# Kernel optimization log

Hardware: AMD Instinct MI355X
Metric: run time of the kernel (lower is better)

## Reference

```python
import jax, jax.numpy as jnp
import numpy as np

N_NODES = 50000
N_GRAPHS = 128
HEADS = 10
F_XD = 78


def _linear(x, W, b):
    return x @ W + b


def _conv1d(x, w, b):
    # x: [B, Cin, L], w: [Cout, Cin, K]
    y = jax.lax.conv_general_dilated(x, w, (1,), 'VALID',
                                     dimension_numbers=('NCH', 'OIH', 'NCH'))
    return y + b[None, :, None]


def _add_self_loops(src, dst, n):
    loop = jnp.arange(n, dtype=src.dtype)
    return jnp.concatenate([src, loop]), jnp.concatenate([dst, loop])


def _gat_conv(x, src, dst, W, att_src, att_dst, b, n):
    # PyG GATConv, concat heads, self-loops, negative_slope=0.2
    h = (x @ W).reshape(n, HEADS, F_XD)               # [N,H,F]
    a_s = jnp.sum(h * att_src[None], axis=-1)          # [N,H]
    a_d = jnp.sum(h * att_dst[None], axis=-1)          # [N,H]
    e = jax.nn.leaky_relu(a_s[src] + a_d[dst], 0.2)    # [E,H]
    m = jax.ops.segment_max(e, dst, num_segments=n)    # [N,H]
    m = jnp.where(jnp.isfinite(m), m, 0.0)
    ex = jnp.exp(e - m[dst])
    s = jax.ops.segment_sum(ex, dst, num_segments=n)
    alpha = ex / (s[dst] + 1e-16)                      # [E,H]
    out = jax.ops.segment_sum(h[src] * alpha[:, :, None], dst, num_segments=n)
    return out.reshape(n, HEADS * F_XD) + b


def _gcn_conv(x, src, dst, W, b, n):
    # PyG GCNConv: self-loops + symmetric normalization
    h = x @ W                                          # [N,C]
    ones = jnp.ones(src.shape[0], dtype=h.dtype)
    deg = jax.ops.segment_sum(ones, dst, num_segments=n)
    dinv = jnp.where(deg > 0, jax.lax.rsqrt(deg), 0.0)
    norm = dinv[src] * dinv[dst]                       # [E]
    out = jax.ops.segment_sum(h[src] * norm[:, None], dst, num_segments=n)
    return out + b


def _forward(x, edge_index, batch, target1, target2, params):
    p = params
    n = x.shape[0]
    src0, dst0 = edge_index[0], edge_index[1]
    src, dst = _add_self_loops(src0, dst0, n)

    h = jax.nn.relu(_gat_conv(x, src, dst, p['W_gat'], p['att_src'], p['att_dst'], p['b_gat'], n))
    h = jax.nn.relu(_gcn_conv(h, src, dst, p['W_gcn'], p['b_gcn'], n))

    # global max + mean pool per graph
    cnt = jax.ops.segment_sum(jnp.ones(n, dtype=h.dtype), batch, num_segments=N_GRAPHS)
    gmx = jax.ops.segment_max(h, batch, num_segments=N_GRAPHS)
    gmx = jnp.where(cnt[:, None] > 0, gmx, 0.0)
    gav = jax.ops.segment_sum(h, batch, num_segments=N_GRAPHS) / jnp.maximum(cnt, 1.0)[:, None]
    g = jnp.concatenate([gmx, gav], axis=1)            # [B,1560]

    g = jax.nn.relu(_linear(g, p['W_fcg1'], p['b_fcg1']))  # dropout = identity (eval)
    g = _linear(g, p['W_fcg2'], p['b_fcg2'])               # [B,128]

    # protein branch 2: embedding + conv1d over embed dim
    emb = p['emb'][target2]                            # [B,1000,128]
    xt2 = _conv1d(emb, p['Wc2'], p['bc2'])             # [B,32,121]
    xt2 = _linear(xt2.reshape(xt2.shape[0], 32 * 121), p['W_fc2xt'], p['b_fc2xt'])

    # protein branch 1: conv1d on raw float features
    xt1 = _conv1d(target1, p['Wc1'], p['bc1'])         # [B,32,17]
    xt1 = _linear(xt1.reshape(xt1.shape[0], 544), p['W_fc1xt'], p['b_fc1xt'])

    xc = jnp.concatenate([g, xt1, xt2], axis=1)        # [B,384]
    xc = jax.nn.relu(_linear(xc, p['W_fc1'], p['b_fc1']))
    xc = jax.nn.relu(_linear(xc, p['W_fc2'], p['b_fc2']))
    return _linear(xc, p['W_out'], p['b_out'])         # [B,1]


def setup_inputs() -> dict:
    key = jax.random.key(0)
    ks = jax.random.split(key, 32)

    def w(k, shape, fan_in):
        return jax.random.normal(k, shape, dtype=jnp.float32) * (1.0 / np.sqrt(fan_in))

    inp = {}
    inp['x'] = jax.random.normal(ks[0], (N_NODES, F_XD), dtype=jnp.float32)
    inp['edge_index'] = jax.random.randint(ks[1], (2, 150000), 0, N_NODES, dtype=jnp.int64) if jax.config.jax_enable_x64 else jax.random.randint(ks[1], (2, 150000), 0, N_NODES).astype(jnp.int32)
    inp['batch'] = jnp.sort(jax.random.randint(ks[2], (N_NODES,), 0, N_GRAPHS)).astype(jnp.int32)
    inp['target1'] = jax.random.normal(ks[3], (N_GRAPHS, 20, 24), dtype=jnp.float32)
    inp['target2'] = jax.random.randint(ks[4], (N_GRAPHS, 1000), 0, 26).astype(jnp.int32)

    inp['W_gat'] = w(ks[5], (F_XD, HEADS * F_XD), F_XD)
    inp['att_src'] = w(ks[6], (HEADS, F_XD), F_XD)
    inp['att_dst'] = w(ks[7], (HEADS, F_XD), F_XD)
    inp['b_gat'] = jnp.zeros((HEADS * F_XD,), jnp.float32)
    inp['W_gcn'] = w(ks[8], (780, 780), 780)
    inp['b_gcn'] = jnp.zeros((780,), jnp.float32)
    inp['W_fcg1'] = w(ks[9], (1560, 1500), 1560)
    inp['b_fcg1'] = jnp.zeros((1500,), jnp.float32)
    inp['W_fcg2'] = w(ks[10], (1500, 128), 1500)
    inp['b_fcg2'] = jnp.zeros((128,), jnp.float32)
    inp['emb'] = jax.random.normal(ks[11], (26, 128), dtype=jnp.float32)
    inp['Wc2'] = w(ks[12], (32, 1000, 8), 1000 * 8)
    inp['bc2'] = jnp.zeros((32,), jnp.float32)
    inp['W_fc2xt'] = w(ks[13], (32 * 121, 128), 32 * 121)
    inp['b_fc2xt'] = jnp.zeros((128,), jnp.float32)
    inp['Wc1'] = w(ks[14], (32, 20, 8), 20 * 8)
    inp['bc1'] = jnp.zeros((32,), jnp.float32)
    inp['W_fc1xt'] = w(ks[15], (544, 128), 544)
    inp['b_fc1xt'] = jnp.zeros((128,), jnp.float32)
    inp['W_fc1'] = w(ks[16], (384, 1024), 384)
    inp['b_fc1'] = jnp.zeros((1024,), jnp.float32)
    inp['W_fc2'] = w(ks[17], (1024, 512), 1024)
    inp['b_fc2'] = jnp.zeros((512,), jnp.float32)
    inp['W_out'] = w(ks[18], (512, 1), 512)
    inp['b_out'] = jnp.zeros((1,), jnp.float32)
    return inp


def reference(x, edge_index, batch, target1, target2,
              W_gat, att_src, att_dst, b_gat, W_gcn, b_gcn,
              W_fcg1, b_fcg1, W_fcg2, b_fcg2, emb, Wc2, bc2,
              W_fc2xt, b_fc2xt, Wc1, bc1, W_fc1xt, b_fc1xt,
              W_fc1, b_fc1, W_fc2, b_fc2, W_out, b_out):
    params = dict(W_gat=W_gat, att_src=att_src, att_dst=att_dst, b_gat=b_gat,
                  W_gcn=W_gcn, b_gcn=b_gcn, W_fcg1=W_fcg1, b_fcg1=b_fcg1,
                  W_fcg2=W_fcg2, b_fcg2=b_fcg2, emb=emb, Wc2=Wc2, bc2=bc2,
                  W_fc2xt=W_fc2xt, b_fc2xt=b_fc2xt, Wc1=Wc1, bc1=bc1,
                  W_fc1xt=W_fc1xt, b_fc1xt=b_fc1xt, W_fc1=W_fc1, b_fc1=b_fc1,
                  W_fc2=W_fc2, b_fc2=b_fc2, W_out=W_out, b_out=b_out)
    return _forward(x, edge_index, batch, target1, target2, params)
```

## Files before the change

### kernel.cpp

```cpp
#include <hip/hip_runtime.h>
#include <cstdio>
#include <cstdint>

#define CDIV(a,b) (((a)+(b)-1)/(b))

static const int N   = 50000;
static const int NE0 = 150000;
static const int NE  = 200000;
static const int H   = 10;
static const int F   = 78;
static const int C   = 780;
static const int G   = 128;
static const int KP_GAT = 96;
static const int XAGG_LD = 960;
static const int CP1 = 800;
static const int CP1A = 832;
static const int CP2 = 784;
static const int POOL_SPLIT = 8;
static const int BM_SPLIT = 4;

typedef __attribute__((ext_vector_type(8))) short bf16x8;
typedef __attribute__((ext_vector_type(4))) float f32x4;
typedef __attribute__((ext_vector_type(8))) unsigned short us8;

__device__ __forceinline__ float bf2f(unsigned short u) {
    return __uint_as_float(((unsigned int)u) << 16);
}
__device__ __forceinline__ unsigned short f2bf(float f) {
    unsigned int u = __float_as_uint(f);
    u = (u + 0x7fff + ((u >> 16) & 1)) >> 16;
    return (unsigned short)u;
}

__device__ __forceinline__ void async16(const unsigned short* g, unsigned short* l) {
    __builtin_amdgcn_global_load_lds(
        (const __attribute__((address_space(1))) unsigned int*)g,
        (__attribute__((address_space(3))) unsigned int*)l, 16, 0, 0);
}

__global__ __launch_bounds__(256)
void gemm_mfma64(const unsigned short* __restrict__ A,
                 const unsigned short* __restrict__ Bt,
                 unsigned short* __restrict__ Cb,
                 const float* __restrict__ bias, int relu,
                 int M, int Nn, int kSteps, int lda, int ldb, int ldc, int nct)
{
    __shared__ unsigned short As[128][64];
    __shared__ unsigned short Bs[128][64];
    const int tid  = threadIdx.x;
    const int lane = tid & 63;
    const int wave = tid >> 6;
    const int wm = (wave >> 1) * 64, wn = (wave & 1) * 64;

    const int nwg = gridDim.x;
    const int q8 = nwg >> 3, r8 = nwg & 7;
    const int xcd = blockIdx.x & 7, sub = blockIdx.x >> 3;
    const int wg = (xcd < r8) ? xcd * (q8 + 1) + sub
                              : r8 * (q8 + 1) + (xcd - r8) * q8 + sub;
    const int bm = (wg / nct) * 128, bn = (wg % nct) * 128;

    f32x4 acc[4][4] = {};

    const int mrow = lane & 15, quad = lane >> 4;
    const int srow = wave * 8 + (lane >> 3);
    const int segoff = ((lane & 7) ^ (lane >> 3)) * 8;

    const unsigned short* gA[4];
    const unsigned short* gB[4];
    unsigned short* lA[4];
    unsigned short* lB[4];
#pragma unroll
    for (int c = 0; c < 4; c++) {
        int r = c * 32 + srow;
        gA[c] = A  + (size_t)min(bm + r, M - 1)  * lda + segoff;
        gB[c] = Bt + (size_t)min(bn + r, Nn - 1) * ldb + segoff;
        lA[c] = &As[c * 32 + wave * 8][0];
        lB[c] = &Bs[c * 32 + wave * 8][0];
    }

    for (int ks = 0; ks < kSteps; ks++) {
        const int k0 = ks * 64;
#pragma unroll
        for (int c = 0; c < 4; c++) async16(gA[c] + k0, lA[c]);
#pragma unroll
        for (int c = 0; c < 4; c++) async16(gB[c] + k0, lB[c]);
        __syncthreads();
#pragma unroll
        for (int kk = 0; kk < 2; kk++) {
            bf16x8 af[4], bfr[4];
#pragma unroll
            for (int i = 0; i < 4; i++) {
                int ra = wm + i * 16 + mrow;
                af[i]  = *(const bf16x8*)&As[ra][(((kk * 4 + quad) ^ (ra & 7))) * 8];
                int rb = wn + i * 16 + mrow;
                bfr[i] = *(const bf16x8*)&Bs[rb][(((kk * 4 + quad) ^ (rb & 7))) * 8];
            }
#pragma unroll
            for (int i = 0; i < 4; i++)
#pragma unroll
                for (int j = 0; j < 4; j++)
                    acc[i][j] = __builtin_amdgcn_mfma_f32_16x16x32_bf16(af[i], bfr[j], acc[i][j], 0, 0, 0);
        }
        __syncthreads();
    }

#pragma unroll
    for (int i = 0; i < 4; i++) {
#pragma unroll
        for (int j = 0; j < 4; j++) {
            int col = bn + wn + j * 16 + mrow;
            if (col >= Nn) continue;
            float bv = bias ? bias[col] : 0.f;
#pragma unroll
            for (int r = 0; r < 4; r++) {
                int row = bm + wm + i * 16 + quad * 4 + r;
                if (row >= M) continue;
                float v = acc[i][j][r] + bv;
                if (relu) v = fmaxf(v, 0.f);
                Cb[(size_t)row * ldc + col] = f2bf(v);
            }
        }
    }
}

__global__ __launch_bounds__(256)
void gemm_gat(const unsigned short* __restrict__ A,
              const unsigned short* __restrict__ Bt,
              const float* __restrict__ bias,
              unsigned short* __restrict__ Cb)
{
    __shared__ unsigned short As[128][32];
    __shared__ unsigned short Bs[128][32];
    const int tid  = threadIdx.x;
    const int lane = tid & 63;
    const int wave = tid >> 6;
    const int wm = (wave >> 1) * 64, wn = (wave & 1) * 64;
    const int h = blockIdx.y;

    const int nwg = gridDim.x;
    const int q8 = nwg >> 3, r8 = nwg & 7;
    const int xcd = blockIdx.x & 7, sub = blockIdx.x >> 3;
    const int wg = (xcd < r8) ? xcd * (q8 + 1) + sub
                              : r8 * (q8 + 1) + (xcd - r8) * q8 + sub;
    const int bm = wg * 128;

    f32x4 acc[4][4] = {};

    const int mrow = lane & 15, quad = lane >> 4;
    const int subr = lane >> 2;
    const int segp = ((lane & 3) ^ ((lane >> 3) & 3)) * 8;
    const int segr = (quad ^ ((mrow >> 1) & 3)) * 8;

    const unsigned short* gA0 = A + (size_t)min(bm + wave * 16 + subr,      N - 1) * XAGG_LD + h * KP_GAT + segp;
    const unsigned short* gA1 = A + (size_t)min(bm + 64 + wave * 16 + subr, N - 1) * XAGG_LD + h * KP_GAT + segp;
    const unsigned short* gB0 = Bt + (size_t)(h * 80 + min(wave * 16 + subr,      79)) * KP_GAT + segp;
    const unsigned short* gB1 = Bt + (size_t)(h * 80 + min(64 + wave * 16 + subr, 79)) * KP_GAT + segp;
    unsigned short* lA0 = &As[wave * 16][0];
    unsigned short* lA1 = &As[64 + wave * 16][0];
    unsigned short* lB0 = &Bs[wave * 16][0];
    unsigned short* lB1 = &Bs[64 + wave * 16][0];

#pragma unroll
    for (int ks = 0; ks < 3; ks++) {
        const int k0 = ks * 32;
        async16(gA0 + k0, lA0);
        async16(gA1 + k0, lA1);
        async16(gB0 + k0, lB0);
        async16(gB1 + k0, lB1);
        __syncthreads();
        bf16x8 af[4], bfr[4];
#pragma unroll
        for (int i = 0; i < 4; i++) {
            af[i]  = *(const bf16x8*)&As[wm + i * 16 + mrow][segr];
            bfr[i] = *(const bf16x8*)&Bs[wn + i * 16 + mrow][segr];
        }
#pragma unroll
        for (int i = 0; i < 4; i++)
#pragma unroll
            for (int j = 0; j < 4; j++)
                acc[i][j] = __builtin_amdgcn_mfma_f32_16x16x32_bf16(af[i], bfr[j], acc[i][j], 0, 0, 0);
        __syncthreads();
    }

#pragma unroll
    for (int i = 0; i < 4; i++) {
#pragma unroll
        for (int j = 0; j < 4; j++) {
            int cl = wn + j * 16 + mrow;
            if (cl >= 80) continue;
            float bv = bias[h * 80 + cl];
#pragma unroll
            for (int r = 0; r < 4; r++) {
                int row = bm + wm + i * 16 + quad * 4 + r;
                if (row >= N) continue;
                float v = fmaxf(acc[i][j][r] + bv, 0.f);
                Cb[(size_t)row * CP1A + h * 80 + cl] = f2bf(v);
            }
        }
    }
}

__global__ __launch_bounds__(256)
void gemm_mfma_sk(const unsigned short* __restrict__ A,
                  const unsigned short* __restrict__ Bt,
                  float* __restrict__ Cp,
                  int M, int Nn, int kSteps, int lda, int ldb, int nct)
{
    __shared__ unsigned short As[128][32];
    __shared__ unsigned short Bs[128][32];
    const int tid  = threadIdx.x;
    const int lane = tid & 63;
    const int wave = tid >> 6;
    const int wm = (wave >> 1) * 64, wn = (wave & 1) * 64;
    const int bm = (blockIdx.x / nct) * 128, bn = (blockIdx.x % nct) * 128;

    const int split = blockIdx.y, KS = gridDim.y;
    const int per = CDIV(kSteps, KS);
    const int kb = split * per;
    const int ke = min(kb + per, kSteps);

    f32x4 acc[4][4] = {};

    const int mrow = lane & 15, quad = lane >> 4;
    const int subr = lane >> 2;
    const int segp = ((lane & 3) ^ ((lane >> 3) & 3)) * 8;
    const int segr = (quad ^ ((mrow >> 1) & 3)) * 8;

    const unsigned short* gA0 = A  + (size_t)min(bm + wave * 16 + subr,      M - 1)  * lda + segp;
    const unsigned short* gA1 = A  + (size_t)min(bm + 64 + wave * 16 + subr, M - 1)  * lda + segp;
    const unsigned short* gB0 = Bt + (size_t)min(bn + wave * 16 + subr,      Nn - 1) * ldb + segp;
    const unsigned short* gB1 = Bt + (size_t)min(bn + 64 + wave * 16 + subr, Nn - 1) * ldb + segp;
    unsigned short* lA0 = &As[wave * 16][0];
    unsigned short* lA1 = &As[64 + wave * 16][0];
    unsigned short* lB0 = &Bs[wave * 16][0];
    unsigned short* lB1 = &Bs[64 + wave * 16][0];

    for (int ks = kb; ks < ke; ks++) {
        const int k0 = ks * 32;
        async16(gA0 + k0, lA0);
        async16(gA1 + k0, lA1);
        async16(gB0 + k0, lB0);
        async16(gB1 + k0, lB1);
        __syncthreads();
        bf16x8 af[4], bfr[4];
#pragma unroll
        for (int i = 0; i < 4; i++) {
            af[i]  = *(const bf16x8*)&As[wm + i * 16 + mrow][segr];
            bfr[i] = *(const bf16x8*)&Bs[wn + i * 16 + mrow][segr];
        }
#pragma unroll
        for (int i = 0; i < 4; i++)
#pragma unroll
            for (int j = 0; j < 4; j++)
                acc[i][j] = __builtin_amdgcn_mfma_f32_16x16x32_bf16(af[i], bfr[j], acc[i][j], 0, 0, 0);
        __syncthreads();
    }

    float* Cs = Cp + (size_t)split * M * Nn;
#pragma unroll
    for (int i = 0; i < 4; i++) {
#pragma unroll
        for (int j = 0; j < 4; j++) {
            int col = bn + wn + j * 16 + mrow;
            if (col >= Nn) continue;
#pragma unroll
            for (int r = 0; r < 4; r++) {
                int row = bm + wm + i * 16 + quad * 4 + r;
                if (row >= M) continue;
                Cs[(size_t)row * Nn + col] = acc[i][j][r];
            }
        }
    }
}

__global__ void k_sk_reduce(const float* __restrict__ Cp, int KS, int M, int Nn,
                            const float* __restrict__ bias, int relu,
                            unsigned short* __restrict__ Cb, int ldc)
{
    int idx = blockIdx.x * blockDim.x + threadIdx.x;
    if (idx >= M * Nn) return;
    int row = idx / Nn, col = idx % Nn;
    float v = bias ? bias[col] : 0.f;
    for (int s = 0; s < KS; s++) v += Cp[((size_t)s * M + row) * Nn + col];
    if (relu) v = fmaxf(v, 0.f);
    Cb[(size_t)row * ldc + col] = f2bf(v);
}

__global__ void k_fc_out(const unsigned short* __restrict__ f2, const float* __restrict__ W,
                         const float* __restrict__ b, float* __restrict__ out)
{
    int g = blockIdx.x, lane = threadIdx.x;
    float acc = 0.f;
    for (int k = lane; k < 512; k += 64) acc += bf2f(f2[g * 512 + k]) * W[k];
#pragma unroll
    for (int off = 32; off > 0; off >>= 1) acc += __shfl_down(acc, off, 64);
    if (lane == 0) out[g] = acc + b[0];
}

__global__ void k_cast_pad_x(const float* __restrict__ x, unsigned short* __restrict__ xb)
{
    int idx = blockIdx.x * blockDim.x + threadIdx.x;
    if (idx >= N * KP_GAT) return;
    int n = idx / KP_GAT, k = idx % KP_GAT;
    float v = (k < F) ? x[(size_t)n * F + k] : 0.f;
    xb[idx] = f2bf(v);
}

__global__ void k_transpose_cast_t(const float* __restrict__ W, unsigned short* __restrict__ Wt,
                                   int K, int Nn, int Kpad)
{
    __shared__ float tile[32][33];
    int k0 = blockIdx.x * 32, n0 = blockIdx.y * 32;
    int tx = threadIdx.x, ty = threadIdx.y;
    for (int r = ty; r < 32; r += 8) {
        int k = k0 + r, n = n0 + tx;
        tile[r][tx] = (k < K && n < Nn) ? W[(size_t)k * Nn + n] : 0.f;
    }
    __syncthreads();
    for (int r = ty; r < 32; r += 8) {
        int n = n0 + r, k = k0 + tx;
        if (n < Nn && k < Kpad) Wt[(size_t)n * Kpad + k] = f2bf(tile[tx][r]);
    }
}

__global__ void k_build_Wgat_t(const float* __restrict__ W_gat, unsigned short* __restrict__ Wt)
{
    int idx = blockIdx.x * blockDim.x + threadIdx.x;
    if (idx >= KP_GAT * CP1) return;
    int k = idx / CP1, n = idx % CP1;
    int h = n / 80, f = n % 80;
    float v = (k < F && f < F) ? W_gat[(size_t)k * C + h * F + f] : 0.f;
    Wt[(size_t)n * KP_GAT + k] = f2bf(v);
}

__global__ void k_build_bgat(const float* __restrict__ b_gat, float* __restrict__ bp)
{
    int i = blockIdx.x * blockDim.x + threadIdx.x;
    if (i >= CP1) return;
    int h = i / 80, f = i % 80;
    bp[i] = (f < F) ? b_gat[h * F + f] : 0.f;
}

__global__ void k_build_Wgcn_t(const float* __restrict__ W_gcn, unsigned short* __restrict__ Wt)
{
    int idx = blockIdx.x * blockDim.x + threadIdx.x;
    if (idx >= C * CP2) return;
    int ko = idx / CP2, n = idx % CP2;
    int h = ko / F, f = ko % F;
    float v = (n < C) ? W_gcn[(size_t)ko * C + n] : 0.f;
    Wt[(size_t)n * CP1A + h * 80 + f] = f2bf(v);
}

__global__ void k_Vsd(const float* __restrict__ W_gat, const float* __restrict__ att_src,
                      const float* __restrict__ att_dst, float* __restrict__ V_s,
                      float* __restrict__ V_d)
{
    int idx = blockIdx.x * blockDim.x + threadIdx.x;
    if (idx >= F * H) return;
    int k = idx / H, h = idx % H;
    const float* wr = W_gat + (size_t)k * C + h * F;
    const float* as = att_src + h * F;
    const float* ad = att_dst + h * F;
    float s = 0.f, d = 0.f;
    for (int f = 0; f < F; f++) { float w = wr[f]; s += w * as[f]; d += w * ad[f]; }
    V_s[idx] = s; V_d[idx] = d;
}

__global__ void k_ascores(const float* __restrict__ x, const float* __restrict__ V_s,
                          const float* __restrict__ V_d, float* __restrict__ a_s,
                          float* __restrict__ a_d)
{
    __shared__ float Vs[F * H], Vd[F * H];
    int t = threadIdx.x;
    for (int i = t; i < F * H; i += 256) { Vs[i] = V_s[i]; Vd[i] = V_d[i]; }
    __syncthreads();
    int n = blockIdx.x * 256 + t;
    if (n >= N) return;
    const float* xr = x + (size_t)n * F;
    float accs[H] = {}, accd[H] = {};
    for (int k = 0; k < F; k++) {
        float xv = xr[k];
        const float* vs = &Vs[k * H];
        const float* vd = &Vd[k * H];
#pragma unroll
        for (int h = 0; h < H; h++) { accs[h] += xv * vs[h]; accd[h] += xv * vd[h]; }
    }
    for (int h = 0; h < H; h++) { a_s[n * H + h] = accs[h]; a_d[n * H + h] = accd[h]; }
}

__global__ void count_deg(const int* __restrict__ ei, int* __restrict__ deg)
{
    int e = blockIdx.x * blockDim.x + threadIdx.x;
    if (e >= NE) return;
    int d = (e < NE0) ? ei[NE0 + e] : (e - NE0);
    atomicAdd(&deg[d], 1);
}

__global__ void scan_int(const int* __restrict__ cnt, int* __restrict__ row_start, int n)
{
    __shared__ int partial[1024];
    int tid = threadIdx.x;
    int per = CDIV(n, 1024);
    int start = tid * per, end = min(start + per, n);
    int sum = 0;
    for (int i = start; i < end; i++) sum += cnt[i];
    partial[tid] = sum;
    __syncthreads();
    for (int off = 1; off < 1024; off *= 2) {
        int v = (tid >= off) ? partial[tid - off] : 0;
        __syncthreads();
        partial[tid] += v;
        __syncthreads();
    }
    int base = (tid > 0) ? partial[tid - 1] : 0;
    for (int i = start; i < end; i++) { row_start[i] = base; base += cnt[i]; }
    if (tid == 1023) row_start[n] = base;
}

__global__ void fill_csr_ev(const int* __restrict__ ei, const int* __restrict__ row_start,
                            int* __restrict__ fill_cnt, int* __restrict__ srcs,
                            const float* __restrict__ a_s, const float* __restrict__ a_d,
                            float* __restrict__ evb)
{
    int e = blockIdx.x * blockDim.x + threadIdx.x;
    if (e >= NE) return;
    int sr = (e < NE0) ? ei[e] : (e - NE0);
    int d  = (e < NE0) ? ei[NE0 + e] : (e - NE0);
    int pos = row_start[d] + atomicAdd(&fill_cnt[d], 1);
    srcs[pos] = sr;
    const float* as = a_s + sr * H;
    const float* ad = a_d + d * H;
    float* ev = evb + (size_t)pos * H;
#pragma unroll
    for (int h = 0; h < H; h++) {
        float v = as[h] + ad[h];
        ev[h] = (v > 0.f) ? v : 0.2f * v;
    }
}

__global__ void k_gstart(const int* __restrict__ batch, int* __restrict__ gstart)
{
    int g = blockIdx.x * blockDim.x + threadIdx.x;
    if (g > G) return;
    int lo = 0, hi = N;
    while (lo < hi) {
        int mid = (lo + hi) >> 1;
        if (batch[mid] < g) lo = mid + 1; else hi = mid;
    }
    gstart[g] = lo;
}

__global__ void k_softmax_alpha(const int* __restrict__ row_start, float* __restrict__ evb)
{
    int idx = blockIdx.x * blockDim.x + threadIdx.x;
    if (idx >= N * H) return;
    int n = idx / H, h = idx % H;
    int rs = row_start[n], re = row_start[n + 1];
    float m = -INFINITY, s = 0.f;
    for (int i = rs; i < re; i++) {
        float ev = evb[(size_t)i * H + h];
        if (ev <= m) {
            s += expf(ev - m);
        } else {
            s = s * expf(m - ev) + 1.f;
            m = ev;
        }
    }
    float inv = 1.f / (s + 1e-16f);
    for (int i = rs; i < re; i++) {
        float ev = evb[(size_t)i * H + h];
        evb[(size_t)i * H + h] = expf(ev - m) * inv;
    }
}

__global__ __launch_bounds__(128)
void gat_agg_x(const unsigned short* __restrict__ xb, const float* __restrict__ alpha,
               const int* __restrict__ srcs, const int* __restrict__ row_start,
               unsigned short* __restrict__ xagg)
{
    int n = blockIdx.x;
    int f = threadIdx.x;
    if (f >= KP_GAT) return;
    int rs = row_start[n], re = row_start[n + 1];
    float acc[H] = {};
    for (int i = rs; i < re; i++) {
        int sr = srcs[i];
        float xv = bf2f(xb[(size_t)sr * KP_GAT + f]);
        const float* al = alpha + (size_t)i * H;
#pragma unroll
        for (int h = 0; h < H; h++) acc[h] += al[h] * xv;
    }
#pragma unroll
    for (int h = 0; h < H; h++)
        xagg[(size_t)n * XAGG_LD + h * KP_GAT + f] = f2bf(acc[h]);
}

__global__ void k_zero_tail(unsigned short* __restrict__ gat_out)
{
    int idx = blockIdx.x * blockDim.x + threadIdx.x;
    if (idx >= N * 32) return;
    int n = idx / 32, c = idx % 32;
    gat_out[(size_t)n * CP1A + CP1 + c] = 0;
}

__global__ void k_dinv(const int* __restrict__ deg, float* __restrict__ dinv)
{
    int n = blockIdx.x * blockDim.x + threadIdx.x;
    if (n >= N) return;
    int d = deg[n];
    dinv[n] = (d > 0) ? 1.f / sqrtf((float)d) : 0.f;
}

__global__ __launch_bounds__(128)
void gcn_agg(const unsigned short* __restrict__ h2, const float* __restrict__ dinv,
             const int* __restrict__ srcs, const int* __restrict__ row_start,
             const float* __restrict__ b_gcn, unsigned short* __restrict__ out)
{
    int n = blockIdx.x;
    int c = threadIdx.x * 8;
    if (c >= CP2) return;
    float dn = dinv[n];
    int rs = row_start[n], re = row_start[n + 1];
    float acc[8] = {};
    for (int i = rs; i < re; i++) {
        int sr = srcs[i];
        float d = dinv[sr];
        us8 v = *(const us8*)&h2[(size_t)sr * CP2 + c];
#pragma unroll
        for (int j = 0; j < 8; j++) acc[j] += d * bf2f(v[j]);
    }
    us8 o;
#pragma unroll
    for (int j = 0; j < 8; j++) {
        int col = c + j;
        float r = (col < C) ? fmaxf(acc[j] * dn + b_gcn[col], 0.f) : 0.f;
        o[j] = f2bf(r);
    }
    *(us8*)&out[(size_t)n * CP2 + c] = o;
}

__global__ __launch_bounds__(128)
void k_pool(const unsigned short* __restrict__ hh, const int* __restrict__ gstart,
            float* __restrict__ gfeat)
{
    int g = blockIdx.x;
    int c = threadIdx.x * 8;
    if (c >= CP2) return;
    int s0 = gstart[g], e0 = gstart[g + 1];
    int len = e0 - s0;
    if (len <= 0) return;
    int per = CDIV(len, (int)gridDim.y);
    int s = s0 + (int)blockIdx.y * per;
    int e = min(s + per, e0);
    if (s >= e) return;
    float mx[8] = {}, sm[8] = {};
    for (int n = s; n < e; n++) {
        us8 v = *(const us8*)&hh[(size_t)n * CP2 + c];
#pragma unroll
        for (int j = 0; j < 8; j++) { float f = bf2f(v[j]); mx[j] = fmaxf(mx[j], f); sm[j] += f; }
    }
#pragma unroll
    for (int j = 0; j < 8; j++) {
        int col = c + j;
        if (col < C) {
            atomicMax((unsigned int*)&gfeat[g * 1560 + col], __float_as_uint(mx[j]));
            atomicAdd(&gfeat[g * 1560 + 780 + col], sm[j]);
        }
    }
}

__global__ void k_pool_cast(const float* __restrict__ gfeat, const int* __restrict__ gstart,
                            unsigned short* __restrict__ dst)
{
    int idx = blockIdx.x * blockDim.x + threadIdx.x;
    if (idx >= G * 1568) return;
    int g = idx / 1568, k = idx % 1568;
    float v = 0.f;
    if (k < 780) {
        v = gfeat[g * 1560 + k];
    } else if (k < 1560) {
        float cnt = fmaxf((float)(gstart[g + 1] - gstart[g]), 1.f);
        v = gfeat[g * 1560 + k] * (1.f / cnt);
    }
    dst[idx] = f2bf(v);
}

__global__ void k_build_M(const int* __restrict__ t2, const float* __restrict__ Wc2,
                          float* __restrict__ Mbuf)
{
    __shared__ float Ml[26 * 256];
    int b = blockIdx.x, t = threadIdx.x, s = blockIdx.y;
    for (int j = t; j < 26 * 256; j += 256) Ml[j] = 0.f;
    __syncthreads();
    int o = t >> 3, k = t & 7;
    const int* tb = t2 + b * 1000;
    int c0 = s * (1000 / BM_SPLIT), c1 = c0 + (1000 / BM_SPLIT);
    for (int cc = c0; cc < c1; cc++) {
        int tok = tb[cc];
        Ml[tok * 256 + t] += Wc2[o * 8000 + cc * 8 + k];
    }
    __syncthreads();
    float* Mb = Mbuf + ((size_t)b * BM_SPLIT + s) * (26 * 256);
    for (int j = t; j < 26 * 256; j += 256) Mb[j] = Ml[j];
}

__global__ void k_reduce_M(const float* __restrict__ Mbuf, float* __restrict__ Mfin)
{
    int idx = blockIdx.x * blockDim.x + threadIdx.x;
    if (idx >= G * 26 * 256) return;
    int b = idx / (26 * 256), j = idx % (26 * 256);
    const float* p = Mbuf + (size_t)b * BM_SPLIT * (26 * 256);
    float v = 0.f;
#pragma unroll
    for (int s = 0; s < BM_SPLIT; s++) v += p[(size_t)s * (26 * 256) + j];
    Mfin[idx] = v;
}

__global__ void k_conv2(const float* __restrict__ Mbuf, const float* __restrict__ emb,
                        const float* __restrict__ bc2, unsigned short* __restrict__ xt2c)
{
    int idx = blockIdx.x * blockDim.x + threadIdx.x;
    if (idx >= G * 3872) return;
    int b = idx / 3872, r = idx % 3872;
    int o = r / 121, l = r % 121;
    const float* Mb = Mbuf + (size_t)b * (26 * 256);
    float acc = bc2[o];
    for (int t = 0; t < 26; t++) {
        const float* mrow = Mb + t * 256 + o * 8;
        const float* erow = emb + t * 128 + l;
#pragma unroll
        for (int k = 0; k < 8; k++) acc += mrow[k] * erow[k];
    }
    xt2c[idx] = f2bf(acc);
}

__global__ void k_conv1(const float* __restrict__ t1, const float* __restrict__ Wc1,
                        const float* __restrict__ bc1, unsigned short* __restrict__ xt1c)
{
    int idx = blockIdx.x * blockDim.x + threadIdx.x;
    if (idx >= G * 544) return;
    int b = idx / 544, r = idx % 544;
    int o = r / 17, l = r % 17;
    float acc = bc1[o];
    const float* xb = t1 + b * 480;
    const float* wo = Wc1 + o * 160;
    for (int cc = 0; cc < 20; cc++) {
        const float* xr = xb + cc * 24 + l;
        const float* wr = wo + cc * 8;
#pragma unroll
        for (int k = 0; k < 8; k++) acc += xr[k] * wr[k];
    }
    xt1c[idx] = f2bf(acc);
}

extern "C" void kernel_launch(void* const* d_in, const int* in_sizes, int n_in,
                              void* d_out, int out_size, void* d_ws, size_t ws_size,
                              hipStream_t stream)
{
    const float* x       = (const float*)d_in[0];
    const int*   ei      = (const int*)  d_in[1];
    const int*   batch   = (const int*)  d_in[2];
    const float* t1      = (const float*)d_in[3];
    const int*   t2      = (const int*)  d_in[4];
    const float* W_gat   = (const float*)d_in[5];
    const float* att_src = (const float*)d_in[6];
    const float* att_dst = (const float*)d_in[7];
    const float* b_gat   = (const float*)d_in[8];
    const float* W_gcn   = (const float*)d_in[9];
    const float* b_gcn   = (const float*)d_in[10];
    const float* W_fcg1  = (const float*)d_in[11];
    const float* b_fcg1  = (const float*)d_in[12];
    const float* W_fcg2  = (const float*)d_in[13];
    const float* b_fcg2  = (const float*)d_in[14];
    const float* emb     = (const float*)d_in[15];
    const float* Wc2     = (const float*)d_in[16];
    const float* bc2     = (const float*)d_in[17];
    const float* W_fc2xt = (const float*)d_in[18];
    const float* b_fc2xt = (const float*)d_in[19];
    const float* Wc1     = (const float*)d_in[20];
    const float* bc1     = (const float*)d_in[21];
    const float* W_fc1xt = (const float*)d_in[22];
    const float* b_fc1xt = (const float*)d_in[23];
    const float* W_fc1   = (const float*)d_in[24];
    const float* b_fc1   = (const float*)d_in[25];
    const float* W_fc2   = (const float*)d_in[26];
    const float* b_fc2   = (const float*)d_in[27];
    const float* W_out   = (const float*)d_in[28];
    const float* b_out   = (const float*)d_in[29];

    char* wsb = (char*)d_ws;
    size_t off = 0;
    auto alloc = [&](size_t bytes) -> char* {
        char* p = wsb + off;
        off += (bytes + 255) & ~(size_t)255;
        return p;
    };

    unsigned short* h_buf   = (unsigned short*)alloc((size_t)N * XAGG_LD * 2);
    unsigned short* gat_out = (unsigned short*)alloc((size_t)N * CP1A * 2);
    unsigned short* xb      = (unsigned short*)alloc((size_t)N * KP_GAT * 2);
    unsigned short* Wgat_t  = (unsigned short*)alloc((size_t)CP1 * KP_GAT * 2);
    unsigned short* Wgcn_t  = (unsigned short*)alloc((size_t)CP2 * CP1A * 2);
    unsigned short* Wfcg1_t  = (unsigned short*)alloc((size_t)1500 * 1568 * 2);
    unsigned short* Wfcg2_t  = (unsigned short*)alloc((size_t)128 * 1504 * 2);
    unsigned short* Wfc2xt_t = (unsigned short*)alloc((size_t)128 * 3872 * 2);
    unsigned short* Wfc1xt_t = (unsigned short*)alloc((size_t)128 * 544 * 2);
    unsigned short* Wfc1_t   = (unsigned short*)alloc((size_t)1024 * 384 * 2);
    unsigned short* Wfc2_t   = (unsigned short*)alloc((size_t)512 * 1024 * 2);
    unsigned short* gfeat_b  = (unsigned short*)alloc((size_t)G * 1568 * 2);
    unsigned short* g1_b     = (unsigned short*)alloc((size_t)G * 1504 * 2);
    unsigned short* xt2c_b   = (unsigned short*)alloc((size_t)G * 3872 * 2);
    unsigned short* xt1c_b   = (unsigned short*)alloc((size_t)G * 544 * 2);
    unsigned short* xc_b     = (unsigned short*)alloc((size_t)G * 384 * 2);
    unsigned short* f1_b     = (unsigned short*)alloc((size_t)G * 1024 * 2);
    unsigned short* f2_b     = (unsigned short*)alloc((size_t)G * 512 * 2);
    float* skbuf  = (float*)alloc((size_t)4 * G * 1500 * 4);
    float* bgat_p = (float*)alloc((size_t)CP1 * 4);
    float* V_s    = (float*)alloc((size_t)F * H * 4);
    float* V_d    = (float*)alloc((size_t)F * H * 4);
    float* a_s    = (float*)alloc((size_t)N * H * 4);
    float* a_d    = (float*)alloc((size_t)N * H * 4);
    float* evb    = (float*)alloc((size_t)NE * H * 4);
    float* dinv   = (float*)alloc((size_t)N * 4);
    float* gfeat  = (float*)alloc((size_t)G * 1560 * 4);
    float* Mbuf   = (float*)alloc((size_t)G * BM_SPLIT * 26 * 256 * 4);
    float* Mfin   = (float*)alloc((size_t)G * 26 * 256 * 4);
    int* deg       = (int*)alloc((size_t)N * 4);
    int* row_start = (int*)alloc((size_t)(N + 1) * 4);
    int* fill_cnt  = (int*)alloc((size_t)N * 4);
    int* srcs      = (int*)alloc((size_t)NE * 4);
    int* gstart    = (int*)alloc((size_t)(G + 1) * 4);

    if (off > ws_size) {
        fprintf(stderr, "kernel_launch: workspace too small: need %zu have %zu\n", off, ws_size);
        return;
    }

    hipMemsetAsync(deg, 0, (size_t)N * 4, stream);
    hipMemsetAsync(fill_cnt, 0, (size_t)N * 4, stream);
    hipMemsetAsync(g1_b, 0, (size_t)G * 1504 * 2, stream);
    hipMemsetAsync(Wgcn_t, 0, (size_t)CP2 * CP1A * 2, stream);
    hipMemsetAsync(gfeat, 0, (size_t)G * 1560 * 4, stream);

    dim3 tb(32, 8);

    k_cast_pad_x<<<CDIV(N * KP_GAT, 256), 256, 0, stream>>>(x, xb);
    k_build_Wgat_t<<<CDIV(KP_GAT * CP1, 256), 256, 0, stream>>>(W_gat, Wgat_t);
    k_build_bgat<<<CDIV(CP1, 256), 256, 0, stream>>>(b_gat, bgat_p);
    k_build_Wgcn_t<<<CDIV(C * CP2, 256), 256, 0, stream>>>(W_gcn, Wgcn_t);
    k_transpose_cast_t<<<dim3(CDIV(1568,32), CDIV(1500,32)), tb, 0, stream>>>(W_fcg1, Wfcg1_t, 1560, 1500, 1568);
    k_transpose_cast_t<<<dim3(CDIV(1504,32), CDIV(128,32)),  tb, 0, stream>>>(W_fcg2, Wfcg2_t, 1500, 128, 1504);
    k_transpose_cast_t<<<dim3(CDIV(3872,32), CDIV(128,32)),  tb, 0, stream>>>(W_fc2xt, Wfc2xt_t, 3872, 128, 3872);
    k_transpose_cast_t<<<dim3(CDIV(544,32),  CDIV(128,32)),  tb, 0, stream>>>(W_fc1xt, Wfc1xt_t, 544, 128, 544);
    k_transpose_cast_t<<<dim3(CDIV(384,32),  CDIV(1024,32)), tb, 0, stream>>>(W_fc1, Wfc1_t, 384, 1024, 384);
    k_transpose_cast_t<<<dim3(CDIV(1024,32), CDIV(512,32)),  tb, 0, stream>>>(W_fc2, Wfc2_t, 1024, 512, 1024);

    k_Vsd<<<CDIV(F * H, 256), 256, 0, stream>>>(W_gat, att_src, att_dst, V_s, V_d);
    k_ascores<<<CDIV(N, 256), 256, 0, stream>>>(x, V_s, V_d, a_s, a_d);

    count_deg<<<CDIV(NE, 256), 256, 0, stream>>>(ei, deg);
    scan_int<<<1, 1024, 0, stream>>>(deg, row_start, N);
    fill_csr_ev<<<CDIV(NE, 256), 256, 0, stream>>>(ei, row_start, fill_cnt, srcs, a_s, a_d, evb);
    k_gstart<<<1, 256, 0, stream>>>(batch, gstart);

    k_softmax_alpha<<<CDIV(N * H, 256), 256, 0, stream>>>(row_start, evb);
    k_dinv<<<CDIV(N, 256), 256, 0, stream>>>(deg, dinv);

    gat_agg_x<<<N, 128, 0, stream>>>(xb, evb, srcs, row_start, h_buf);
    gemm_gat<<<dim3(CDIV(N, 128), H), 256, 0, stream>>>(h_buf, Wgat_t, bgat_p, gat_out);
    k_zero_tail<<<CDIV(N * 32, 256), 256, 0, stream>>>(gat_out);

    {
        int rt = CDIV(N, 128), nct = CDIV(CP2, 128);
        gemm_mfma64<<<rt * nct, 256, 0, stream>>>(gat_out, Wgcn_t, h_buf, nullptr, 0,
                                                  N, CP2, CP1A / 64, CP1A, CP1A, CP2, nct);
    }
    unsigned short* gcn_out = gat_out;
    gcn_agg<<<N, 128, 0, stream>>>(h_buf, dinv, srcs, row_start, b_gcn, gcn_out);
    k_pool<<<dim3(G, POOL_SPLIT), 128, 0, stream>>>(gcn_out, gstart, gfeat);
    k_pool_cast<<<CDIV(G * 1568, 256), 256, 0, stream>>>(gfeat, gstart, gfeat_b);

    gemm_mfma_sk<<<dim3(CDIV(1500,128), 4), 256, 0, stream>>>(gfeat_b, Wfcg1_t, skbuf,
                                                              G, 1500, 1568/32, 1568, 1568, CDIV(1500,128));
    k_sk_reduce<<<CDIV(G*1500, 256), 256, 0, stream>>>(skbuf, 4, G, 1500, b_fcg1, 1, g1_b, 1504);
    gemm_mfma_sk<<<dim3(1, 8), 256, 0, stream>>>(g1_b, Wfcg2_t, skbuf,
                                                 G, 128, 1504/32, 1504, 1504, 1);
    k_sk_reduce<<<CDIV(G*128, 256), 256, 0, stream>>>(skbuf, 8, G, 128, b_fcg2, 0, xc_b, 384);

    k_build_M<<<dim3(G, BM_SPLIT), 256, 0, stream>>>(t2, Wc2, Mbuf);
    k_reduce_M<<<CDIV(G * 26 * 256, 256), 256, 0, stream>>>(Mbuf, Mfin);
    k_conv2<<<CDIV(G * 3872, 256), 256, 0, stream>>>(Mfin, emb, bc2, xt2c_b);
    gemm_mfma_sk<<<dim3(1, 16), 256, 0, stream>>>(xt2c_b, Wfc2xt_t, skbuf,
                                                  G, 128, 3872/32, 3872, 3872, 1);
    k_sk_reduce<<<CDIV(G*128, 256), 256, 0, stream>>>(skbuf, 16, G, 128, b_fc2xt, 0, xc_b + 256, 384);

    k_conv1<<<CDIV(G * 544, 256), 256, 0, stream>>>(t1, Wc1, bc1, xt1c_b);
    gemm_mfma_sk<<<dim3(1, 4), 256, 0, stream>>>(xt1c_b, Wfc1xt_t, skbuf,
                                                 G, 128, 544/32, 544, 544, 1);
    k_sk_reduce<<<CDIV(G*128, 256), 256, 0, stream>>>(skbuf, 4, G, 128, b_fc1xt, 0, xc_b + 128, 384);

    gemm_mfma_sk<<<dim3(CDIV(1024,128), 4), 256, 0, stream>>>(xc_b, Wfc1_t, skbuf,
                                                              G, 1024, 384/32, 384, 384, CDIV(1024,128));
    k_sk_reduce<<<CDIV(G*1024, 256), 256, 0, stream>>>(skbuf, 4, G, 1024, b_fc1, 1, f1_b, 1024);
    gemm_mfma_sk<<<dim3(CDIV(512,128), 8), 256, 0, stream>>>(f1_b, Wfc2_t, skbuf,
                                                             G, 512, 1024/32, 1024, 1024, CDIV(512,128));
    k_sk_reduce<<<CDIV(G*512, 256), 256, 0, stream>>>(skbuf, 8, G, 512, b_fc2, 1, f2_b, 512);
    k_fc_out<<<G, 64, 0, stream>>>(f2_b, W_out, b_out, (float*)d_out);
}
```

Before: 691.1 us.

## Enlarge GCN GEMM tile to 256x128 with 8 waves, unroll edge aggregation loops

The GCN GEMM now uses 256-row tiles with 512 threads (8 waves), so each B tile loaded into shared memory is reused across twice as many A rows, and B global traffic per output drops. The GAT and GCN neighbor aggregation loops are unrolled by two so two gathered rows are in flight per iteration, raising memory-level parallelism. The larger tile uses more shared memory and fewer workgroups, which may lower occupancy and leave more padding waste on the M edge.

Measured after the change: 657.1 us. -4.9%, faster.

```diff
diff --git a/kernel.cpp b/kernel.cpp
--- a/kernel.cpp
+++ b/kernel.cpp
@@ -38,44 +38,49 @@
         (__attribute__((address_space(3))) unsigned int*)l, 16, 0, 0);
 }
 
-__global__ __launch_bounds__(256)
-void gemm_mfma64(const unsigned short* __restrict__ A,
-                 const unsigned short* __restrict__ Bt,
-                 unsigned short* __restrict__ Cb,
-                 const float* __restrict__ bias, int relu,
-                 int M, int Nn, int kSteps, int lda, int ldb, int ldc, int nct)
-{
-    __shared__ unsigned short As[128][64];
+__global__ __launch_bounds__(512)
+void gemm_mfma_256(const unsigned short* __restrict__ A,
+                   const unsigned short* __restrict__ Bt,
+                   unsigned short* __restrict__ Cb,
+                   const float* __restrict__ bias, int relu,
+                   int M, int Nn, int kSteps, int lda, int ldb, int ldc, int nct)
+{
+    __shared__ unsigned short As[256][64];
     __shared__ unsigned short Bs[128][64];
     const int tid  = threadIdx.x;
     const int lane = tid & 63;
     const int wave = tid >> 6;
-    const int wm = (wave >> 1) * 64, wn = (wave & 1) * 64;
+    const int wm = (wave >> 1) * 64;
+    const int wn = (wave & 1) * 64;
 
     const int nwg = gridDim.x;
     const int q8 = nwg >> 3, r8 = nwg & 7;
     const int xcd = blockIdx.x & 7, sub = blockIdx.x >> 3;
     const int wg = (xcd < r8) ? xcd * (q8 + 1) + sub
                               : r8 * (q8 + 1) + (xcd - r8) * q8 + sub;
-    const int bm = (wg / nct) * 128, bn = (wg % nct) * 128;
+    const int bm = (wg / nct) * 256, bn = (wg % nct) * 128;
 
     f32x4 acc[4][4] = {};
 
     const int mrow = lane & 15, quad = lane >> 4;
-    const int srow = wave * 8 + (lane >> 3);
+    const int srow = lane >> 3;
     const int segoff = ((lane & 7) ^ (lane >> 3)) * 8;
 
     const unsigned short* gA[4];
-    const unsigned short* gB[4];
     unsigned short* lA[4];
-    unsigned short* lB[4];
 #pragma unroll
     for (int c = 0; c < 4; c++) {
-        int r = c * 32 + srow;
-        gA[c] = A  + (size_t)min(bm + r, M - 1)  * lda + segoff;
+        int r = c * 64 + wave * 8 + srow;
+        gA[c] = A + (size_t)min(bm + r, M - 1) * lda + segoff;
+        lA[c] = &As[c * 64 + wave * 8][0];
+    }
+    const unsigned short* gB[2];
+    unsigned short* lB[2];
+#pragma unroll
+    for (int c = 0; c < 2; c++) {
+        int r = c * 64 + wave * 8 + srow;
         gB[c] = Bt + (size_t)min(bn + r, Nn - 1) * ldb + segoff;
-        lA[c] = &As[c * 32 + wave * 8][0];
-        lB[c] = &Bs[c * 32 + wave * 8][0];
+        lB[c] = &Bs[c * 64 + wave * 8][0];
     }
 
     for (int ks = 0; ks < kSteps; ks++) {
@@ -83,7 +88,7 @@
 #pragma unroll
         for (int c = 0; c < 4; c++) async16(gA[c] + k0, lA[c]);
 #pragma unroll
-        for (int c = 0; c < 4; c++) async16(gB[c] + k0, lB[c]);
+        for (int c = 0; c < 2; c++) async16(gB[c] + k0, lB[c]);
         __syncthreads();
 #pragma unroll
         for (int kk = 0; kk < 2; kk++) {
@@ -483,7 +488,17 @@
     if (f >= KP_GAT) return;
     int rs = row_start[n], re = row_start[n + 1];
     float acc[H] = {};
-    for (int i = rs; i < re; i++) {
+    int i = rs;
+    for (; i + 1 < re; i += 2) {
+        int sr0 = srcs[i], sr1 = srcs[i + 1];
+        float xv0 = bf2f(xb[(size_t)sr0 * KP_GAT + f]);
+        float xv1 = bf2f(xb[(size_t)sr1 * KP_GAT + f]);
+        const float* al0 = alpha + (size_t)i * H;
+        const float* al1 = alpha + (size_t)(i + 1) * H;
+#pragma unroll
+        for (int h = 0; h < H; h++) acc[h] += al0[h] * xv0 + al1[h] * xv1;
+    }
+    if (i < re) {
         int sr = srcs[i];
         float xv = bf2f(xb[(size_t)sr * KP_GAT + f]);
         const float* al = alpha + (size_t)i * H;
@@ -522,7 +537,16 @@
     float dn = dinv[n];
     int rs = row_start[n], re = row_start[n + 1];
     float acc[8] = {};
-    for (int i = rs; i < re; i++) {
+    int i = rs;
+    for (; i + 1 < re; i += 2) {
+        int sr0 = srcs[i], sr1 = srcs[i + 1];
+        float d0 = dinv[sr0], d1 = dinv[sr1];
+        us8 v0 = *(const us8*)&h2[(size_t)sr0 * CP2 + c];
+        us8 v1 = *(const us8*)&h2[(size_t)sr1 * CP2 + c];
+#pragma unroll
+        for (int j = 0; j < 8; j++) acc[j] += d0 * bf2f(v0[j]) + d1 * bf2f(v1[j]);
+    }
+    if (i < re) {
         int sr = srcs[i];
         float d = dinv[sr];
         us8 v = *(const us8*)&h2[(size_t)sr * CP2 + c];
@@ -771,9 +795,9 @@
     k_zero_tail<<<CDIV(N * 32, 256), 256, 0, stream>>>(gat_out);
 
     {
-        int rt = CDIV(N, 128), nct = CDIV(CP2, 128);
-        gemm_mfma64<<<rt * nct, 256, 0, stream>>>(gat_out, Wgcn_t, h_buf, nullptr, 0,
-                                                  N, CP2, CP1A / 64, CP1A, CP1A, CP2, nct);
+        int rt = CDIV(N, 256), nct = CDIV(CP2, 128);
+        gemm_mfma_256<<<rt * nct, 512, 0, stream>>>(gat_out, Wgcn_t, h_buf, nullptr, 0,
+                                                    N, CP2, CP1A / 64, CP1A, CP1A, CP2, nct);
     }
     unsigned short* gcn_out = gat_out;
     gcn_agg<<<N, 128, 0, stream>>>(h_buf, dinv, srcs, row_start, b_gcn, gcn_out);
```
